# Optimization experiments

Hardware: AMD Instinct MI355X
Metric: run time of the kernel (lower is better)

The kernel has to match this reference:

```python
import jax, jax.numpy as jnp
import numpy as np

B = 128          # batch
D = 2048         # original_dim
P = 16000        # projection_dim


def _count_sketch_matrix(key, d, p):
    """Dense count-sketch matrix: one +/-1 per row at a random column.
    Mirrors the torch init: col ~ randint(0, p-1), sign = 2*randint(0,2)-1."""
    k_idx, k_sgn = jax.random.split(key)
    idx = jax.random.randint(k_idx, (d,), 0, p - 1)            # torch uses high=p-1 (exclusive)
    sgn = (2 * jax.random.randint(k_sgn, (d,), 0, 2) - 1).astype(jnp.float32)
    C = jnp.zeros((d, p), dtype=jnp.float32)
    return C.at[jnp.arange(d), idx].set(sgn)


def setup_inputs() -> dict:
    key = jax.random.key(0)
    kx1, kx2, kc1, kc2 = jax.random.split(key, 4)
    x1 = jax.random.normal(kx1, (B, D), dtype=jnp.float32)
    x2 = jax.random.normal(kx2, (B, D), dtype=jnp.float32)
    C1 = _count_sketch_matrix(kc1, D, P)
    C2 = _count_sketch_matrix(kc2, D, P)
    return {"x1": x1, "x2": x2, "C1": C1, "C2": C2}


def reference(x1, x2, C1, C2):
    # Count-sketch projections (dense mm, as in the original module)
    y1 = x1 @ C1                      # [B, P]
    y2 = x2 @ C2                      # [B, P]
    # Circular convolution via FFT -> elementwise complex multiply -> IFFT.
    # Original takes only the real part of the IFFT output.
    f1 = jnp.fft.fft(y1, axis=-1)
    f2 = jnp.fft.fft(y2, axis=-1)
    phi = jnp.fft.ifft(f1 * f2, axis=-1).real.astype(jnp.float32)
    return phi                        # [B, P]
```

## Files before the change

### kernel.cpp

```cpp
#include <hip/hip_runtime.h>

#define NFFT 16000
#define BATCH 128
#define DIM 2048
#define TP 17

__device__ __forceinline__ float2 cmul(float2 a, float2 b) {
    return make_float2(a.x * b.x - a.y * b.y, a.x * b.y + a.y * b.x);
}
__device__ __forceinline__ float2 cadd(float2 a, float2 b) { return make_float2(a.x + b.x, a.y + b.y); }
__device__ __forceinline__ float2 csub(float2 a, float2 b) { return make_float2(a.x - b.x, a.y - b.y); }
__device__ __forceinline__ float2 cis(float ang) { return make_float2(__cosf(ang), __sinf(ang)); }

__device__ __forceinline__ int rev5_3(int n) {
    int d0 = n % 5, r = n / 5;
    int d1 = r % 5, d2 = r / 5;
    return d0 * 25 + d1 * 5 + d2;
}
__device__ __forceinline__ int rev7(int x) { return (int)(__brev((unsigned)x) >> 25); }

__device__ __forceinline__ float2 shfl2(float2 v, int lane) {
    return make_float2(__shfl(v.x, lane), __shfl(v.y, lane));
}
__device__ __forceinline__ float2 shfl2_xor(float2 v, int mask) {
    return make_float2(__shfl_xor(v.x, mask), __shfl_xor(v.y, mask));
}

__device__ __forceinline__ float2 conjG(float2 Zk, float2 Zm) {
    float u = (Zk.x * Zk.x - Zk.y * Zk.y) - (Zm.x * Zm.x - Zm.y * Zm.y);
    float v = 2.f * (Zk.x * Zk.y + Zm.x * Zm.y);
    return make_float2(0.25f * v, 0.25f * u);
}

__device__ __forceinline__ void dif128(float2& x0, float2& x1, const float2* tw, int l) {
    {
        float2 a = x0, b = x1;
        x0 = cadd(a, b);
        x1 = cmul(csub(a, b), tw[0]);
    }
    int s = 1;
    #pragma unroll
    for (int m = 32; m >= 1; m >>= 1, ++s) {
        float2 w = tw[s];
        float2 o0 = shfl2_xor(x0, m), o1 = shfl2_xor(x1, m);
        if (l & m) {
            x0 = cmul(csub(o0, x0), w);
            x1 = cmul(csub(o1, x1), w);
        } else {
            x0 = cadd(x0, o0);
            x1 = cadd(x1, o1);
        }
    }
}

__global__ void extract_sketch(const float* __restrict__ C1, const float* __restrict__ C2,
                               int* __restrict__ idx1, float* __restrict__ sgn1,
                               int* __restrict__ idx2, float* __restrict__ sgn2) {
    int gwave = (blockIdx.x * blockDim.x + threadIdx.x) >> 6;
    int lane = threadIdx.x & 63;
    if (gwave >= 2 * DIM) return;
    const float* row;
    int* idxp; float* sgnp; int d;
    if (gwave < DIM) { d = gwave;       row = C1 + (size_t)d * NFFT; idxp = idx1; sgnp = sgn1; }
    else             { d = gwave - DIM; row = C2 + (size_t)d * NFFT; idxp = idx2; sgnp = sgn2; }
    for (int step = 0; step < 16; ++step) {
        int off0 = step * 1024 + lane * 4;
        float4 v[4];
        #pragma unroll
        for (int c = 0; c < 4; ++c) {
            int off = off0 + c * 256;
            v[c] = (off < NFFT) ? *reinterpret_cast<const float4*>(row + off)
                                : make_float4(0.f, 0.f, 0.f, 0.f);
        }
        bool found = false;
        #pragma unroll
        for (int c = 0; c < 4; ++c) {
            float4 w = v[c];
            if (w.x != 0.f || w.y != 0.f || w.z != 0.f || w.w != 0.f) {
                int off = off0 + c * 256;
                int j; float s;
                if (w.x != 0.f)      { j = 0; s = w.x; }
                else if (w.y != 0.f) { j = 1; s = w.y; }
                else if (w.z != 0.f) { j = 2; s = w.z; }
                else                 { j = 3; s = w.w; }
                idxp[d] = off + j;
                sgnp[d] = s;
                found = true;
            }
        }
        if (__any(found)) return;
    }
}

__global__ void __launch_bounds__(512) k1_colfft(
        const float* __restrict__ x1, const float* __restrict__ x2,
        const int* __restrict__ idx1, const float* __restrict__ sgn1,
        const int* __restrict__ idx2, const float* __restrict__ sgn2,
        float2* __restrict__ U) {
    __shared__ float2 S[32 * 125];
    const int b = blockIdx.x >> 2, q = blockIdx.x & 3;
    const int tid = threadIdx.x;

    for (int i = tid; i < 32 * 125; i += 512) S[i] = make_float2(0.f, 0.f);
    __syncthreads();

    const float* x1b = x1 + (size_t)b * DIM;
    const float* x2b = x2 + (size_t)b * DIM;
    for (int d = tid; d < DIM; d += 512) {
        int p1 = idx1[d]; int n1a = p1 & 127;
        if ((n1a >> 5) == q) atomicAdd(&S[(n1a & 31) * 125 + rev5_3(p1 >> 7)].x, sgn1[d] * x1b[d]);
        int p2 = idx2[d]; int n1b = p2 & 127;
        if ((n1b >> 5) == q) atomicAdd(&S[(n1b & 31) * 125 + rev5_3(p2 >> 7)].y, sgn2[d] * x2b[d]);
    }
    __syncthreads();

    const float C1_5 = 0.30901699437494742f, S1_5 = 0.95105651629515357f;
    const float C2_5 = -0.80901699437494745f, S2_5 = 0.58778525229247312f;
    const float2 w5tab[5] = { make_float2(1.f, 0.f),
                              make_float2(C1_5, -S1_5), make_float2(C2_5, -S2_5),
                              make_float2(C2_5,  S2_5), make_float2(C1_5,  S1_5) };
    #pragma unroll
    for (int s = 0; s < 3; ++s) {
        const int m = (s == 0) ? 1 : (s == 1) ? 5 : 25;
        const float angstep = -6.28318530717958647692f / (float)(5 * m);
        for (int task = tid; task < 32 * 25; task += 512) {
            int row = task / 25;
            int bf = task - row * 25;
            int t = bf % m, blk = bf / m;
            int base = row * 125 + blk * (5 * m) + t;
            float2 xv[5];
            #pragma unroll
            for (int r = 0; r < 5; ++r) xv[r] = S[base + r * m];
            if (m > 1) {
                float2 w1 = cis(angstep * (float)t);
                float2 w2 = cmul(w1, w1), w3 = cmul(w2, w1), w4 = cmul(w2, w2);
                xv[1] = cmul(xv[1], w1); xv[2] = cmul(xv[2], w2);
                xv[3] = cmul(xv[3], w3); xv[4] = cmul(xv[4], w4);
            }
            float2 y[5];
            #pragma unroll
            for (int qq = 0; qq < 5; ++qq) {
                float2 acc = xv[0];
                #pragma unroll
                for (int r = 1; r < 5; ++r) {
                    float2 t2 = cmul(xv[r], w5tab[(qq * r) % 5]);
                    acc.x += t2.x; acc.y += t2.y;
                }
                y[qq] = acc;
            }
            #pragma unroll
            for (int qq = 0; qq < 5; ++qq) S[base + qq * m] = y[qq];
        }
        __syncthreads();
    }

    const float ANGN = -6.28318530717958647692f / 16000.0f;
    const int n1base = q * 32;
    float2* Ub = U + (size_t)b * NFFT;
    for (int i = tid; i < 32 * 125; i += 512) {
        int n1l = i & 31, k2 = i >> 5;
        int n1 = n1base + n1l;
        Ub[k2 * 128 + n1] = cmul(S[n1l * 125 + k2], cis(ANGN * (float)(n1 * k2)));
    }
}

__global__ void __launch_bounds__(256) k2_pair(const float2* __restrict__ U,
                                               float2* __restrict__ V) {
    const int w = threadIdx.x >> 6, l = threadIdx.x & 63;
    const int task = blockIdx.x * 4 + w;
    const int b = task / 63, cg = task - b * 63;
    const int c = cg, cm = cg ? 125 - cg : 0;
    const float2* Ub = U + (size_t)b * NFFT;
    const float PI_F = 3.14159265358979323846f;

    float2 tw[7];
    tw[0] = cis(-PI_F / 64.0f * (float)l);
    {
        int m = 32;
        #pragma unroll
        for (int s = 1; s < 7; ++s, m >>= 1)
            tw[s] = cis(-PI_F / (float)m * (float)(l & (m - 1)));
    }

    float2 a0 = Ub[c * 128 + l], a1 = Ub[c * 128 + l + 64];
    dif128(a0, a1, tw, l);
    float2 b0, b1;
    if (cg) {
        b0 = Ub[cm * 128 + l]; b1 = Ub[cm * 128 + l + 64];
        dif128(b0, b1, tw, l);
    }

    const int e  = rev7(l);
    const int lp = rev7(126 - e);

    float2 gA0, gA1, gB0, gB1;
    if (cg) {
        float2 zm0 = shfl2(b1, lp);
        float2 zm1 = shfl2(b0, lp);
        gA0 = conjG(a0, zm0);
        gA1 = conjG(a1, zm1);
        float2 ym0 = shfl2(a1, lp);
        float2 ym1 = shfl2(a0, lp);
        gB0 = conjG(b0, ym0);
        gB1 = conjG(b1, ym1);
    } else {
        int hz = rev7((128 - e) & 127);
        float2 zm0 = shfl2(a0, hz);
        float2 zm1 = shfl2(a1, lp);
        gA0 = conjG(a0, zm0);
        gA1 = conjG(a1, zm1);
        gB0 = gB1 = make_float2(0.f, 0.f);
    }

    const int q = rev7(l & 62);
    const float ANGN = -6.28318530717958647692f / 16000.0f;
    float2* Vb = V + (size_t)b * NFFT;

    {
        float2 t00 = shfl2(gA0, q),     t10 = shfl2(gA1, q);
        float2 t01 = shfl2(gA0, q + 1), t11 = shfl2(gA1, q + 1);
        float2 p0 = (l & 1) ? t10 : t00;
        float2 p1 = (l & 1) ? t11 : t01;
        dif128(p0, p1, tw, l);
        p0 = cmul(p0, cis(ANGN * (float)(c * e)));
        p1 = cmul(p1, cis(ANGN * (float)(c * (e + 1))));
        *reinterpret_cast<float4*>(&Vb[c * 128 + e]) = make_float4(p0.x, p0.y, p1.x, p1.y);
    }
    if (cg) {
        float2 t00 = shfl2(gB0, q),     t10 = shfl2(gB1, q);
        float2 t01 = shfl2(gB0, q + 1), t11 = shfl2(gB1, q + 1);
        float2 p0 = (l & 1) ? t10 : t00;
        float2 p1 = (l & 1) ? t11 : t01;
        dif128(p0, p1, tw, l);
        p0 = cmul(p0, cis(ANGN * (float)(cm * e)));
        p1 = cmul(p1, cis(ANGN * (float)(cm * (e + 1))));
        *reinterpret_cast<float4*>(&Vb[cm * 128 + e]) = make_float4(p0.x, p0.y, p1.x, p1.y);
    }
}

__global__ void __launch_bounds__(256) k3_rowfft(const float2* __restrict__ V,
                                                 float* __restrict__ out) {
    __shared__ float2 T[125 * TP];
    const int b = blockIdx.x >> 3, g = blockIdx.x & 7;
    const int j1base = g * 16, tid = threadIdx.x;
    const float2* Vb = V + (size_t)b * NFFT;

    for (int i = tid; i < 125 * 16; i += 256) {
        int m1 = i >> 4, j1l = i & 15;
        T[rev5_3(m1) * TP + j1l] = Vb[m1 * 128 + j1base + j1l];
    }
    __syncthreads();

    const float C1_5 = 0.30901699437494742f, S1_5 = 0.95105651629515357f;
    const float C2_5 = -0.80901699437494745f, S2_5 = 0.58778525229247312f;
    const float2 w5tab[5] = { make_float2(1.f, 0.f),
                              make_float2(C1_5, -S1_5), make_float2(C2_5, -S2_5),
                              make_float2(C2_5,  S2_5), make_float2(C1_5,  S1_5) };
    #pragma unroll
    for (int s = 0; s < 3; ++s) {
        const int m = (s == 0) ? 1 : (s == 1) ? 5 : 25;
        const float angstep = -6.28318530717958647692f / (float)(5 * m);
        for (int task = tid; task < 16 * 25; task += 256) {
            int bf = task >> 4;
            int j1l = task & 15;
            int t = bf % m, blk = bf / m;
            int base = (blk * (5 * m) + t) * TP + j1l;
            float2 xv[5];
            #pragma unroll
            for (int r = 0; r < 5; ++r) xv[r] = T[base + r * m * TP];
            if (m > 1) {
                float2 w1 = cis(angstep * (float)t);
                float2 w2 = cmul(w1, w1), w3 = cmul(w2, w1), w4 = cmul(w2, w2);
                xv[1] = cmul(xv[1], w1); xv[2] = cmul(xv[2], w2);
                xv[3] = cmul(xv[3], w3); xv[4] = cmul(xv[4], w4);
            }
            float2 y[5];
            #pragma unroll
            for (int qq = 0; qq < 5; ++qq) {
                float2 acc = xv[0];
                #pragma unroll
                for (int r = 1; r < 5; ++r) {
                    float2 t2 = cmul(xv[r], w5tab[(qq * r) % 5]);
                    acc.x += t2.x; acc.y += t2.y;
                }
                y[qq] = acc;
            }
            #pragma unroll
            for (int qq = 0; qq < 5; ++qq) T[base + qq * m * TP] = y[qq];
        }
        __syncthreads();
    }

    const float invN = 1.0f / (float)NFFT;
    float* outb = out + (size_t)b * NFFT;
    for (int i = tid; i < 125 * 16; i += 256) {
        int j2 = i >> 4, j1l = i & 15;
        outb[j1base + j1l + 128 * j2] = T[j2 * TP + j1l].x * invN;
    }
}

extern "C" void kernel_launch(void* const* d_in, const int* in_sizes, int n_in,
                              void* d_out, int out_size, void* d_ws, size_t ws_size,
                              hipStream_t stream) {
    (void)in_sizes; (void)n_in; (void)out_size; (void)ws_size;
    const float* x1 = (const float*)d_in[0];
    const float* x2 = (const float*)d_in[1];
    const float* C1 = (const float*)d_in[2];
    const float* C2 = (const float*)d_in[3];
    float* out = (float*)d_out;

    char* w = (char*)d_ws;
    int*    idx1 = (int*)  (w);
    float*  sgn1 = (float*)(w + 8192);
    int*    idx2 = (int*)  (w + 16384);
    float*  sgn2 = (float*)(w + 24576);
    float2* U    = (float2*)(w + 32768);
    float2* V    = (float2*)(w + 32768 + 16384000);

    extract_sketch<<<(2 * DIM) / 4, 256, 0, stream>>>(C1, C2, idx1, sgn1, idx2, sgn2);
    k1_colfft     <<<BATCH * 4, 512, 0, stream>>>(x1, x2, idx1, sgn1, idx2, sgn2, U);
    k2_pair       <<<2016, 256, 0, stream>>>(U, V);
    k3_rowfft     <<<BATCH * 8, 256, 0, stream>>>(V, out);
}
```

Measured before the change: 296.2 us.

## Fuse column FFT, pair combine and row IFFT into one per-batch LDS kernel

Merges the three FFT kernels into a single kernel with one 1024-thread block per batch row that keeps the whole 16000-point complex buffer (128 KB) in LDS. The scattered sketch, the radix-5 column FFTs, the 128-point paired FFTs and the inverse radix-5 row FFTs all run in shared memory, and the last inverse stage is switched to decimation-in-frequency so output comes out in digit-reversed order that the final store undoes. This removes the global round trips through the U and V workspaces and two kernel launches. In exchange only 128 blocks run, each using a large LDS allocation, which limits occupancy to about one block per CU. The in-LDS column accesses at stride 125 may also cause bank conflicts.

```diff
diff --git a/kernel.cpp b/kernel.cpp
--- a/kernel.cpp
+++ b/kernel.cpp
@@ -3,7 +3,6 @@
 #define NFFT 16000
 #define BATCH 128
 #define DIM 2048
-#define TP 17
 
 __device__ __forceinline__ float2 cmul(float2 a, float2 b) {
     return make_float2(a.x * b.x - a.y * b.y, a.x * b.y + a.y * b.x);
@@ -92,25 +91,25 @@
     }
 }
 
-__global__ void __launch_bounds__(512) k1_colfft(
+__global__ void __launch_bounds__(1024) fused_fft(
         const float* __restrict__ x1, const float* __restrict__ x2,
         const int* __restrict__ idx1, const float* __restrict__ sgn1,
         const int* __restrict__ idx2, const float* __restrict__ sgn2,
-        float2* __restrict__ U) {
-    __shared__ float2 S[32 * 125];
-    const int b = blockIdx.x >> 2, q = blockIdx.x & 3;
+        float* __restrict__ out) {
+    __shared__ float2 A[16000];
+    const int b = blockIdx.x;
     const int tid = threadIdx.x;
 
-    for (int i = tid; i < 32 * 125; i += 512) S[i] = make_float2(0.f, 0.f);
+    for (int i = tid; i < 16000; i += 1024) A[i] = make_float2(0.f, 0.f);
     __syncthreads();
 
     const float* x1b = x1 + (size_t)b * DIM;
     const float* x2b = x2 + (size_t)b * DIM;
-    for (int d = tid; d < DIM; d += 512) {
-        int p1 = idx1[d]; int n1a = p1 & 127;
-        if ((n1a >> 5) == q) atomicAdd(&S[(n1a & 31) * 125 + rev5_3(p1 >> 7)].x, sgn1[d] * x1b[d]);
-        int p2 = idx2[d]; int n1b = p2 & 127;
-        if ((n1b >> 5) == q) atomicAdd(&S[(n1b & 31) * 125 + rev5_3(p2 >> 7)].y, sgn2[d] * x2b[d]);
+    for (int d = tid; d < DIM; d += 1024) {
+        int p1 = idx1[d];
+        atomicAdd(&A[(p1 & 127) * 125 + rev5_3(p1 >> 7)].x, sgn1[d] * x1b[d]);
+        int p2 = idx2[d];
+        atomicAdd(&A[(p2 & 127) * 125 + rev5_3(p2 >> 7)].y, sgn2[d] * x2b[d]);
     }
     __syncthreads();
 
@@ -119,18 +118,19 @@
     const float2 w5tab[5] = { make_float2(1.f, 0.f),
                               make_float2(C1_5, -S1_5), make_float2(C2_5, -S2_5),
                               make_float2(C2_5,  S2_5), make_float2(C1_5,  S1_5) };
+
     #pragma unroll
     for (int s = 0; s < 3; ++s) {
         const int m = (s == 0) ? 1 : (s == 1) ? 5 : 25;
         const float angstep = -6.28318530717958647692f / (float)(5 * m);
-        for (int task = tid; task < 32 * 25; task += 512) {
+        for (int task = tid; task < 128 * 25; task += 1024) {
             int row = task / 25;
             int bf = task - row * 25;
             int t = bf % m, blk = bf / m;
             int base = row * 125 + blk * (5 * m) + t;
             float2 xv[5];
             #pragma unroll
-            for (int r = 0; r < 5; ++r) xv[r] = S[base + r * m];
+            for (int r = 0; r < 5; ++r) xv[r] = A[base + r * m];
             if (m > 1) {
                 float2 w1 = cis(angstep * (float)t);
                 float2 w2 = cmul(w1, w1), w3 = cmul(w2, w1), w4 = cmul(w2, w2);
@@ -149,29 +149,14 @@
                 y[qq] = acc;
             }
             #pragma unroll
-            for (int qq = 0; qq < 5; ++qq) S[base + qq * m] = y[qq];
+            for (int qq = 0; qq < 5; ++qq) A[base + qq * m] = y[qq];
         }
         __syncthreads();
     }
 
+    const int w = tid >> 6, l = tid & 63;
+    const float PI_F = 3.14159265358979323846f;
     const float ANGN = -6.28318530717958647692f / 16000.0f;
-    const int n1base = q * 32;
-    float2* Ub = U + (size_t)b * NFFT;
-    for (int i = tid; i < 32 * 125; i += 512) {
-        int n1l = i & 31, k2 = i >> 5;
-        int n1 = n1base + n1l;
-        Ub[k2 * 128 + n1] = cmul(S[n1l * 125 + k2], cis(ANGN * (float)(n1 * k2)));
-    }
-}
-
-__global__ void __launch_bounds__(256) k2_pair(const float2* __restrict__ U,
-                                               float2* __restrict__ V) {
-    const int w = threadIdx.x >> 6, l = threadIdx.x & 63;
-    const int task = blockIdx.x * 4 + w;
-    const int b = task / 63, cg = task - b * 63;
-    const int c = cg, cm = cg ? 125 - cg : 0;
-    const float2* Ub = U + (size_t)b * NFFT;
-    const float PI_F = 3.14159265358979323846f;
 
     float2 tw[7];
     tw[0] = cis(-PI_F / 64.0f * (float)l);
@@ -182,98 +167,80 @@
             tw[s] = cis(-PI_F / (float)m * (float)(l & (m - 1)));
     }
 
-    float2 a0 = Ub[c * 128 + l], a1 = Ub[c * 128 + l + 64];
-    dif128(a0, a1, tw, l);
-    float2 b0, b1;
-    if (cg) {
-        b0 = Ub[cm * 128 + l]; b1 = Ub[cm * 128 + l + 64];
-        dif128(b0, b1, tw, l);
-    }
-
-    const int e  = rev7(l);
-    const int lp = rev7(126 - e);
-
-    float2 gA0, gA1, gB0, gB1;
-    if (cg) {
-        float2 zm0 = shfl2(b1, lp);
-        float2 zm1 = shfl2(b0, lp);
-        gA0 = conjG(a0, zm0);
-        gA1 = conjG(a1, zm1);
-        float2 ym0 = shfl2(a1, lp);
-        float2 ym1 = shfl2(a0, lp);
-        gB0 = conjG(b0, ym0);
-        gB1 = conjG(b1, ym1);
-    } else {
-        int hz = rev7((128 - e) & 127);
-        float2 zm0 = shfl2(a0, hz);
-        float2 zm1 = shfl2(a1, lp);
-        gA0 = conjG(a0, zm0);
-        gA1 = conjG(a1, zm1);
-        gB0 = gB1 = make_float2(0.f, 0.f);
-    }
-
-    const int q = rev7(l & 62);
-    const float ANGN = -6.28318530717958647692f / 16000.0f;
-    float2* Vb = V + (size_t)b * NFFT;
-
-    {
-        float2 t00 = shfl2(gA0, q),     t10 = shfl2(gA1, q);
-        float2 t01 = shfl2(gA0, q + 1), t11 = shfl2(gA1, q + 1);
-        float2 p0 = (l & 1) ? t10 : t00;
-        float2 p1 = (l & 1) ? t11 : t01;
-        dif128(p0, p1, tw, l);
-        p0 = cmul(p0, cis(ANGN * (float)(c * e)));
-        p1 = cmul(p1, cis(ANGN * (float)(c * (e + 1))));
-        *reinterpret_cast<float4*>(&Vb[c * 128 + e]) = make_float4(p0.x, p0.y, p1.x, p1.y);
-    }
-    if (cg) {
-        float2 t00 = shfl2(gB0, q),     t10 = shfl2(gB1, q);
-        float2 t01 = shfl2(gB0, q + 1), t11 = shfl2(gB1, q + 1);
-        float2 p0 = (l & 1) ? t10 : t00;
-        float2 p1 = (l & 1) ? t11 : t01;
-        dif128(p0, p1, tw, l);
-        p0 = cmul(p0, cis(ANGN * (float)(cm * e)));
-        p1 = cmul(p1, cis(ANGN * (float)(cm * (e + 1))));
-        *reinterpret_cast<float4*>(&Vb[cm * 128 + e]) = make_float4(p0.x, p0.y, p1.x, p1.y);
-    }
-}
-
-__global__ void __launch_bounds__(256) k3_rowfft(const float2* __restrict__ V,
-                                                 float* __restrict__ out) {
-    __shared__ float2 T[125 * TP];
-    const int b = blockIdx.x >> 3, g = blockIdx.x & 7;
-    const int j1base = g * 16, tid = threadIdx.x;
-    const float2* Vb = V + (size_t)b * NFFT;
-
-    for (int i = tid; i < 125 * 16; i += 256) {
-        int m1 = i >> 4, j1l = i & 15;
-        T[rev5_3(m1) * TP + j1l] = Vb[m1 * 128 + j1base + j1l];
+    for (int tsk = w; tsk < 63; tsk += 16) {
+        const int c = tsk, cm = tsk ? 125 - tsk : 0;
+
+        float2 a0 = cmul(A[l * 125 + c],        cis(ANGN * (float)(l * c)));
+        float2 a1 = cmul(A[(l + 64) * 125 + c], cis(ANGN * (float)((l + 64) * c)));
+        dif128(a0, a1, tw, l);
+        float2 b0, b1;
+        if (tsk) {
+            b0 = cmul(A[l * 125 + cm],        cis(ANGN * (float)(l * cm)));
+            b1 = cmul(A[(l + 64) * 125 + cm], cis(ANGN * (float)((l + 64) * cm)));
+            dif128(b0, b1, tw, l);
+        }
+
+        const int e  = rev7(l);
+        const int lp = rev7(126 - e);
+
+        float2 gA0, gA1, gB0, gB1;
+        if (tsk) {
+            float2 zm0 = shfl2(b1, lp);
+            float2 zm1 = shfl2(b0, lp);
+            gA0 = conjG(a0, zm0);
+            gA1 = conjG(a1, zm1);
+            float2 ym0 = shfl2(a1, lp);
+            float2 ym1 = shfl2(a0, lp);
+            gB0 = conjG(b0, ym0);
+            gB1 = conjG(b1, ym1);
+        } else {
+            int hz = rev7((128 - e) & 127);
+            float2 zm0 = shfl2(a0, hz);
+            float2 zm1 = shfl2(a1, lp);
+            gA0 = conjG(a0, zm0);
+            gA1 = conjG(a1, zm1);
+            gB0 = gB1 = make_float2(0.f, 0.f);
+        }
+
+        const int q = rev7(l & 62);
+        {
+            float2 t00 = shfl2(gA0, q),     t10 = shfl2(gA1, q);
+            float2 t01 = shfl2(gA0, q + 1), t11 = shfl2(gA1, q + 1);
+            float2 p0 = (l & 1) ? t10 : t00;
+            float2 p1 = (l & 1) ? t11 : t01;
+            dif128(p0, p1, tw, l);
+            p0 = cmul(p0, cis(ANGN * (float)(c * e)));
+            p1 = cmul(p1, cis(ANGN * (float)(c * (e + 1))));
+            A[e * 125 + c] = p0;
+            A[(e + 1) * 125 + c] = p1;
+        }
+        if (tsk) {
+            float2 t00 = shfl2(gB0, q),     t10 = shfl2(gB1, q);
+            float2 t01 = shfl2(gB0, q + 1), t11 = shfl2(gB1, q + 1);
+            float2 p0 = (l & 1) ? t10 : t00;
+            float2 p1 = (l & 1) ? t11 : t01;
+            dif128(p0, p1, tw, l);
+            p0 = cmul(p0, cis(ANGN * (float)(cm * e)));
+            p1 = cmul(p1, cis(ANGN * (float)(cm * (e + 1))));
+            A[e * 125 + cm] = p0;
+            A[(e + 1) * 125 + cm] = p1;
+        }
     }
     __syncthreads();
 
-    const float C1_5 = 0.30901699437494742f, S1_5 = 0.95105651629515357f;
-    const float C2_5 = -0.80901699437494745f, S2_5 = 0.58778525229247312f;
-    const float2 w5tab[5] = { make_float2(1.f, 0.f),
-                              make_float2(C1_5, -S1_5), make_float2(C2_5, -S2_5),
-                              make_float2(C2_5,  S2_5), make_float2(C1_5,  S1_5) };
     #pragma unroll
     for (int s = 0; s < 3; ++s) {
-        const int m = (s == 0) ? 1 : (s == 1) ? 5 : 25;
-        const float angstep = -6.28318530717958647692f / (float)(5 * m);
-        for (int task = tid; task < 16 * 25; task += 256) {
-            int bf = task >> 4;
-            int j1l = task & 15;
+        const int L = (s == 0) ? 125 : (s == 1) ? 25 : 5;
+        const int m = L / 5;
+        const float angstep = -6.28318530717958647692f / (float)L;
+        for (int task = tid; task < 128 * 25; task += 1024) {
+            int row = task / 25;
+            int bf = task - row * 25;
             int t = bf % m, blk = bf / m;
-            int base = (blk * (5 * m) + t) * TP + j1l;
+            int base = row * 125 + blk * L + t;
             float2 xv[5];
             #pragma unroll
-            for (int r = 0; r < 5; ++r) xv[r] = T[base + r * m * TP];
-            if (m > 1) {
-                float2 w1 = cis(angstep * (float)t);
-                float2 w2 = cmul(w1, w1), w3 = cmul(w2, w1), w4 = cmul(w2, w2);
-                xv[1] = cmul(xv[1], w1); xv[2] = cmul(xv[2], w2);
-                xv[3] = cmul(xv[3], w3); xv[4] = cmul(xv[4], w4);
-            }
+            for (int r = 0; r < 5; ++r) xv[r] = A[base + r * m];
             float2 y[5];
             #pragma unroll
             for (int qq = 0; qq < 5; ++qq) {
@@ -285,17 +252,23 @@
                 }
                 y[qq] = acc;
             }
-            #pragma unroll
-            for (int qq = 0; qq < 5; ++qq) T[base + qq * m * TP] = y[qq];
+            if (L > 5) {
+                float2 w1 = cis(angstep * (float)t);
+                float2 w2 = cmul(w1, w1), w3 = cmul(w2, w1), w4 = cmul(w2, w2);
+                y[1] = cmul(y[1], w1); y[2] = cmul(y[2], w2);
+                y[3] = cmul(y[3], w3); y[4] = cmul(y[4], w4);
+            }
+            #pragma unroll
+            for (int qq = 0; qq < 5; ++qq) A[base + qq * m] = y[qq];
         }
         __syncthreads();
     }
 
     const float invN = 1.0f / (float)NFFT;
     float* outb = out + (size_t)b * NFFT;
-    for (int i = tid; i < 125 * 16; i += 256) {
-        int j2 = i >> 4, j1l = i & 15;
-        outb[j1base + j1l + 128 * j2] = T[j2 * TP + j1l].x * invN;
+    for (int i = tid; i < 16000; i += 1024) {
+        int j1 = i & 127, s = i >> 7;
+        outb[j1 + 128 * rev5_3(s)] = A[j1 * 125 + s].x * invN;
     }
 }
 
@@ -314,11 +287,7 @@
     float*  sgn1 = (float*)(w + 8192);
     int*    idx2 = (int*)  (w + 16384);
     float*  sgn2 = (float*)(w + 24576);
-    float2* U    = (float2*)(w + 32768);
-    float2* V    = (float2*)(w + 32768 + 16384000);
 
     extract_sketch<<<(2 * DIM) / 4, 256, 0, stream>>>(C1, C2, idx1, sgn1, idx2, sgn2);
-    k1_colfft     <<<BATCH * 4, 512, 0, stream>>>(x1, x2, idx1, sgn1, idx2, sgn2, U);
-    k2_pair       <<<2016, 256, 0, stream>>>(U, V);
-    k3_rowfft     <<<BATCH * 8, 256, 0, stream>>>(V, out);
-}
+    fused_fft     <<<BATCH, 1024, 0, stream>>>(x1, x2, idx1, sgn1, idx2, sgn2, out);
+}
```

Measured after the change: 311.5 us. +5.2%, slower.
